# Kernel tuning notes

Hardware: AMD Instinct MI355X
Metric: run time of the kernel (lower is better)

The kernel has to match this reference:

```python
import jax, jax.numpy as jnp
import numpy as np

B, S, A, H, E = 8192, 256, 64, 1024, 8
IN = S + A
OUT = S + 1


def setup_inputs() -> dict:
    key = jax.random.key(0)
    ks = jax.random.split(key, 8)
    state = jax.random.normal(ks[0], (B, S), dtype=jnp.float32)
    action = jax.random.normal(ks[1], (B, A), dtype=jnp.float32)
    idx = jax.random.randint(ks[2], (B,), 0, E, dtype=jnp.int32)
    # Kaiming-ish scaling to keep activations sane
    W1 = jax.random.normal(ks[3], (E, IN, H), dtype=jnp.float32) / np.sqrt(IN)
    b1 = jnp.zeros((E, H), dtype=jnp.float32)
    W2 = jax.random.normal(ks[4], (E, H, H), dtype=jnp.float32) / np.sqrt(H)
    b2 = jnp.zeros((E, H), dtype=jnp.float32)
    W3 = jax.random.normal(ks[5], (E, H, OUT), dtype=jnp.float32) / np.sqrt(H)
    b3 = jnp.zeros((E, OUT), dtype=jnp.float32)
    return {"state": state, "action": action, "idx": idx,
            "W1": W1, "b1": b1, "W2": W2, "b2": b2, "W3": W3, "b3": b3}


def reference(state, action, idx, W1, b1, W2, b2, W3, b3):
    # Dense-MoE style: run all E experts on the full batch, then select the
    # per-sample expert output chosen by idx (matches masked gather/scatter
    # in the torch predict loop).
    x = jnp.concatenate([state, action], axis=-1)                  # [B, IN]
    h = jax.nn.relu(jnp.einsum('bi,eih->beh', x, W1) + b1)         # [B, E, H]
    h = jax.nn.relu(jnp.einsum('beh,ehk->bek', h, W2) + b2)        # [B, E, H]
    out = jnp.einsum('beh,eho->beo', h, W3) + b3                   # [B, E, S+1]
    sel = jnp.take_along_axis(out, idx[:, None, None], axis=1)[:, 0]  # [B, S+1]
    s_dim = state.shape[-1]
    delta = sel[:, :s_dim]
    reward = sel[:, s_dim:]
    next_state = state + delta
    return next_state, reward
```

## Files before the change

kernel.cpp:

```cpp
#include <hip/hip_runtime.h>
#include <stdint.h>

#define B_SZ   8192
#define IN_DIM 320
#define H_DIM  1024
#define E_NUM  8
#define OUT_DIM 257
#define TM     128
#define MAXT   (B_SZ / TM + E_NUM)
#define W3ROWS 384

typedef __bf16 bf16x8 __attribute__((ext_vector_type(8)));
typedef float  f32x4  __attribute__((ext_vector_type(4)));

typedef unsigned int __attribute__((address_space(1))) as1_uint;
typedef unsigned int __attribute__((address_space(3))) as3_uint;

__device__ __forceinline__ void gload_lds16(const void* g, void* l) {
    __builtin_amdgcn_global_load_lds((const as1_uint*)g, (as3_uint*)l, 16, 0, 0);
}

__device__ __forceinline__ unsigned short f2bf(float f) {
    unsigned int u = __float_as_uint(f);
    return (unsigned short)((u + 0x7fffu + ((u >> 16) & 1u)) >> 16);
}

__global__ __launch_bounds__(256)
void k_prep(const float* __restrict__ state, const float* __restrict__ action,
            const int* __restrict__ idx,
            const float* __restrict__ W1, const float* __restrict__ W2,
            const float* __restrict__ W3,
            unsigned short* __restrict__ xb, unsigned short* __restrict__ w1t,
            unsigned short* __restrict__ w2t, unsigned short* __restrict__ w3t,
            int* __restrict__ order, int* __restrict__ te,
            int* __restrict__ tp0, int* __restrict__ tcnt) {
    __shared__ float tile[64][65];
    __shared__ int scnt[16][E_NUM];
    int bid = blockIdx.x, tid = threadIdx.x;

    if (bid == 0) {
        int shard = tid & 15;
        if (tid < 128) ((int*)scnt)[tid] = 0;
        __syncthreads();
        for (int b = tid; b < B_SZ; b += 256) atomicAdd(&scnt[shard][idx[b]], 1);
        __syncthreads();
        if (tid == 0) {
            int pos = 0, tt = 0;
            for (int e = 0; e < E_NUM; e++) {
                int start = pos;
                for (int s = 0; s < 16; s++) { int c = scnt[s][e]; scnt[s][e] = pos; pos += c; }
                int tot = pos - start;
                for (int st = 0; st < tot; st += TM) {
                    te[tt] = e; tp0[tt] = start + st; tcnt[tt] = min(TM, tot - st); tt++;
                }
            }
            for (; tt < MAXT; tt++) { te[tt] = 0; tp0[tt] = 0; tcnt[tt] = 0; }
        }
        __syncthreads();
        for (int b = tid; b < B_SZ; b += 256) {
            int e = idx[b];
            int p = atomicAdd(&scnt[shard][e], 1);
            order[p] = b;
        }
        return;
    }

    if (bid <= 2560) {
        int q = (bid - 1) * 256 + tid;
        int b = q / 80, j = q % 80;
        float4 v = (j < 64) ? ((const float4*)state)[b * 64 + j]
                            : ((const float4*)action)[b * 16 + (j - 64)];
        ushort4 o;
        o.x = f2bf(v.x); o.y = f2bf(v.y); o.z = f2bf(v.z); o.w = f2bf(v.w);
        ((ushort4*)xb)[q] = o;
        return;
    }

    if (bid < 5761) {
        int e, kt, nt, K, Nsrc, dstRows;
        const float* src; unsigned short* dst;
        if (bid < 3201) {
            int r = bid - 2561; e = r / 80; int m = r % 80; kt = m / 16; nt = m % 16;
            K = IN_DIM; Nsrc = H_DIM; dstRows = H_DIM; src = W1; dst = w1t;
        } else if (bid < 5249) {
            int r = bid - 3201; e = r / 256; int m = r % 256; kt = m / 16; nt = m % 16;
            K = H_DIM; Nsrc = H_DIM; dstRows = H_DIM; src = W2; dst = w2t;
        } else {
            int r = bid - 5249; e = r / 64; int m = r % 64; kt = m / 4; nt = m % 4;
            K = H_DIM; Nsrc = OUT_DIM; dstRows = W3ROWS; src = W3; dst = w3t;
        }
        int k0 = kt * 64, n0 = nt * 64;
        const float* s = src + (size_t)e * K * Nsrc;
        unsigned short* d = dst + (size_t)e * dstRows * K;
        int tx = tid & 63, ty = tid >> 6;
        for (int rr = ty; rr < 64; rr += 4)
            tile[rr][tx] = s[(size_t)(k0 + rr) * Nsrc + (n0 + tx)];
        __syncthreads();
        for (int rr = ty; rr < 64; rr += 4)
            d[(size_t)(n0 + rr) * K + (k0 + tx)] = f2bf(tile[tx][rr]);
        return;
    }

    int i = (bid - 5761) * 256 + tid;
    int e = i >> 10, k = i & 1023;
    w3t[((size_t)e * W3ROWS + 256) * H_DIM + k] =
        f2bf(W3[((size_t)e * H_DIM + k) * OUT_DIM + 256]);
}

template <int K, bool GATHER, int MODE>
__global__ __launch_bounds__(256, 2)
void k_gemm(const unsigned short* __restrict__ Abase,
            const unsigned short* __restrict__ Wt, int wtRows,
            const float* __restrict__ bias, int bstride,
            unsigned short* __restrict__ Hout,
            float* __restrict__ Out, const float* __restrict__ state,
            const int* __restrict__ order,
            const int* __restrict__ te, const int* __restrict__ tp0,
            const int* __restrict__ tcnt) {
    constexpr int NI  = K / 32;
    constexpr int ABY = 128 * 64;
    constexpr int STG = 2 * ABY;
    __shared__ __align__(16) char lds[2 * STG];

    int t = blockIdx.x;
    int cnt = tcnt[t];
    if (cnt == 0) return;
    int e = te[t], p0 = tp0[t];
    int n0 = blockIdx.y * 128;
    int tid = threadIdx.x;
    int w = tid >> 6, lane = tid & 63;

    int r  = tid >> 2;
    int cg = (tid & 3) ^ ((r >> 1) & 3);
    int rc0 = r < cnt ? r : cnt - 1;
    int rc1 = (r + 64) < cnt ? (r + 64) : cnt - 1;
    long ar0 = GATHER ? order[p0 + rc0] : (p0 + rc0);
    long ar1 = GATHER ? order[p0 + rc1] : (p0 + rc1);
    const unsigned short* aP0 = Abase + (size_t)ar0 * K + cg * 8;
    const unsigned short* aP1 = Abase + (size_t)ar1 * K + cg * 8;
    const unsigned short* bP0 = Wt + ((size_t)e * wtRows + n0 + r) * K + cg * 8;
    const unsigned short* bP1 = bP0 + (size_t)64 * K;

    auto stage = [&](int k0, int sb) {
        gload_lds16(aP0 + k0, lds + sb + tid * 16);
        gload_lds16(aP1 + k0, lds + sb + 4096 + tid * 16);
        gload_lds16(bP0 + k0, lds + sb + ABY + tid * 16);
        gload_lds16(bP1 + k0, lds + sb + ABY + 4096 + tid * 16);
    };

    f32x4 acc[4][4];
#pragma unroll
    for (int i = 0; i < 4; i++)
#pragma unroll
        for (int j = 0; j < 4; j++) acc[i][j] = (f32x4)0.f;

    const int m_off = (w >> 1) * 64, n_off = (w & 1) * 64;
    const int fm   = lane & 15;
    const int kc   = lane >> 4;
    const int koff = (kc ^ ((fm >> 1) & 3)) * 8;

    stage(0, 0);
    for (int it = 0; it < NI; ++it) {
        __syncthreads();
        if (it + 1 < NI) stage((it + 1) * 32, ((it + 1) & 1) * STG);
        const unsigned short* As = (const unsigned short*)(lds + (it & 1) * STG);
        const unsigned short* Bs = As + ABY / 2;

        bf16x8 af[4], bf[4];
#pragma unroll
        for (int i = 0; i < 4; i++)
            af[i] = *(const bf16x8*)&As[(m_off + i * 16 + fm) * 32 + koff];
#pragma unroll
        for (int j = 0; j < 4; j++)
            bf[j] = *(const bf16x8*)&Bs[(n_off + j * 16 + fm) * 32 + koff];
#pragma unroll
        for (int i = 0; i < 4; i++)
#pragma unroll
            for (int j = 0; j < 4; j++)
                acc[i][j] = __builtin_amdgcn_mfma_f32_16x16x32_bf16(
                    af[i], bf[j], acc[i][j], 0, 0, 0);
    }

    int col = lane & 15, rq = lane >> 4;
#pragma unroll
    for (int j = 0; j < 4; j++) {
        int n = n0 + n_off + j * 16 + col;
        float bv = (MODE == 0) ? bias[e * bstride + n]
                               : ((n <= 256) ? bias[e * bstride + n] : 0.f);
#pragma unroll
        for (int i = 0; i < 4; i++) {
#pragma unroll
            for (int rr = 0; rr < 4; rr++) {
                int m = m_off + i * 16 + rq * 4 + rr;
                if (m < cnt) {
                    float v = acc[i][j][rr] + bv;
                    if (MODE == 0) {
                        Hout[(size_t)(p0 + m) * H_DIM + n] = f2bf(fmaxf(v, 0.f));
                    } else {
                        int row = order[p0 + m];
                        if (n < 256) {
                            size_t o = (size_t)row * 256 + n;
                            Out[o] = state[o] + v;
                        } else if (n == 256) {
                            Out[(size_t)B_SZ * 256 + row] = v;
                        }
                    }
                }
            }
        }
    }
}

extern "C" void kernel_launch(void* const* d_in, const int* in_sizes, int n_in,
                              void* d_out, int out_size, void* d_ws, size_t ws_size,
                              hipStream_t stream) {
    const float* state  = (const float*)d_in[0];
    const float* action = (const float*)d_in[1];
    const int*   idx    = (const int*)d_in[2];
    const float* W1     = (const float*)d_in[3];
    const float* b1     = (const float*)d_in[4];
    const float* W2     = (const float*)d_in[5];
    const float* b2     = (const float*)d_in[6];
    const float* W3     = (const float*)d_in[7];
    const float* b3     = (const float*)d_in[8];
    float* out = (float*)d_out;

    char* ws = (char*)d_ws;
    size_t off = 0;
    auto alloc = [&](size_t bytes) -> void* {
        void* p = ws + off;
        off = (off + bytes + 255) & ~(size_t)255;
        return p;
    };
    unsigned short* xb  = (unsigned short*)alloc((size_t)B_SZ * IN_DIM * 2);
    unsigned short* w1t = (unsigned short*)alloc((size_t)E_NUM * H_DIM * IN_DIM * 2);
    unsigned short* w2t = (unsigned short*)alloc((size_t)E_NUM * H_DIM * H_DIM * 2);
    unsigned short* w3t = (unsigned short*)alloc((size_t)E_NUM * W3ROWS * H_DIM * 2);
    unsigned short* h1  = (unsigned short*)alloc((size_t)B_SZ * H_DIM * 2);
    unsigned short* h2  = (unsigned short*)alloc((size_t)B_SZ * H_DIM * 2);
    int* order = (int*)alloc(B_SZ * 4);
    int* te    = (int*)alloc(MAXT * 4);
    int* tp0   = (int*)alloc(MAXT * 4);
    int* tcnt  = (int*)alloc(MAXT * 4);

    k_prep<<<5793, 256, 0, stream>>>(state, action, idx, W1, W2, W3,
                                     xb, w1t, w2t, w3t, order, te, tp0, tcnt);

    k_gemm<IN_DIM, true, 0><<<dim3(MAXT, 8), 256, 0, stream>>>(
        xb, w1t, H_DIM, b1, H_DIM, h1, nullptr, nullptr, order, te, tp0, tcnt);
    k_gemm<H_DIM, false, 0><<<dim3(MAXT, 8), 256, 0, stream>>>(
        h1, w2t, H_DIM, b2, H_DIM, h2, nullptr, nullptr, order, te, tp0, tcnt);
    k_gemm<H_DIM, false, 1><<<dim3(MAXT, 3), 256, 0, stream>>>(
        h2, w3t, W3ROWS, b3, OUT_DIM, nullptr, out, state, order, te, tp0, tcnt);
}
```

Baseline: 236.8 us.

## Shrink GEMM tiles to 64x64 single-wave blocks and overlap W2/W3 conversion with layer 1

Result: slower. 272.4 us (+15.0%).

```diff
diff --git a/kernel.cpp b/kernel.cpp
--- a/kernel.cpp
+++ b/kernel.cpp
@@ -6,9 +6,12 @@
 #define H_DIM  1024
 #define E_NUM  8
 #define OUT_DIM 257
-#define TM     128
+#define TM     64
 #define MAXT   (B_SZ / TM + E_NUM)
-#define W3ROWS 384
+#define W3ROWS 320
+#define NG12   (MAXT * 16)
+#define NG3    (MAXT * 5)
+#define NAUX   2568
 
 typedef __bf16 bf16x8 __attribute__((ext_vector_type(8)));
 typedef float  f32x4  __attribute__((ext_vector_type(4)));
@@ -25,16 +28,37 @@
     return (unsigned short)((u + 0x7fffu + ((u >> 16) & 1u)) >> 16);
 }
 
+__device__ __forceinline__ void trans64(const float* __restrict__ src,
+                                        unsigned short* __restrict__ dst,
+                                        int Ks, int Ns, int dR, int e, int kt,
+                                        int nt, unsigned short* sh,
+                                        int tid, int nthr) {
+    int k0 = kt * 64, n0 = nt * 64;
+    const float* s = src + (size_t)e * Ks * Ns + (size_t)k0 * Ns + n0;
+    unsigned short* d = dst + ((size_t)e * dR + n0) * Ks + k0;
+    int tx = tid & 63, wv = tid >> 6, nw = nthr >> 6;
+    for (int rr = wv; rr < 64; rr += nw)
+        sh[rr * 66 + tx] = f2bf(s[(size_t)rr * Ns + tx]);
+    __syncthreads();
+    int kq = tid & 15, nr = (tid >> 4) & 3;
+    for (int p = 0; p < 16 / nw; p++) {
+        int n = (wv + p * nw) * 4 + nr;
+        ushort4 o;
+        o.x = sh[(kq * 4 + 0) * 66 + n];
+        o.y = sh[(kq * 4 + 1) * 66 + n];
+        o.z = sh[(kq * 4 + 2) * 66 + n];
+        o.w = sh[(kq * 4 + 3) * 66 + n];
+        *(ushort4*)&d[(size_t)n * Ks + kq * 4] = o;
+    }
+}
+
 __global__ __launch_bounds__(256)
-void k_prep(const float* __restrict__ state, const float* __restrict__ action,
-            const int* __restrict__ idx,
-            const float* __restrict__ W1, const float* __restrict__ W2,
-            const float* __restrict__ W3,
-            unsigned short* __restrict__ xb, unsigned short* __restrict__ w1t,
-            unsigned short* __restrict__ w2t, unsigned short* __restrict__ w3t,
-            int* __restrict__ order, int* __restrict__ te,
-            int* __restrict__ tp0, int* __restrict__ tcnt) {
-    __shared__ float tile[64][65];
+void k_prep0(const float* __restrict__ state, const float* __restrict__ action,
+             const int* __restrict__ idx, const float* __restrict__ W1,
+             unsigned short* __restrict__ xb, unsigned short* __restrict__ w1t,
+             int* __restrict__ order, int* __restrict__ te,
+             int* __restrict__ tp0, int* __restrict__ tcnt) {
+    __shared__ unsigned short sh[64 * 66];
     __shared__ int scnt[16][E_NUM];
     int bid = blockIdx.x, tid = threadIdx.x;
 
@@ -65,50 +89,29 @@
         return;
     }
 
-    if (bid <= 2560) {
-        int q = (bid - 1) * 256 + tid;
-        int b = q / 80, j = q % 80;
-        float4 v = (j < 64) ? ((const float4*)state)[b * 64 + j]
-                            : ((const float4*)action)[b * 16 + (j - 64)];
-        ushort4 o;
-        o.x = f2bf(v.x); o.y = f2bf(v.y); o.z = f2bf(v.z); o.w = f2bf(v.w);
-        ((ushort4*)xb)[q] = o;
+    if (bid <= 320) {
+        int a = bid - 1;
+        const float4* sf = (const float4*)state;
+        const float4* af = (const float4*)action;
+#pragma unroll
+        for (int p = 0; p < 8; p++) {
+            int q = a * 2048 + p * 256 + tid;
+            int b = q / 80, j = q % 80;
+            float4 v = (j < 64) ? sf[b * 64 + j] : af[b * 16 + (j - 64)];
+            ushort4 o;
+            o.x = f2bf(v.x); o.y = f2bf(v.y); o.z = f2bf(v.z); o.w = f2bf(v.w);
+            ((ushort4*)xb)[q] = o;
+        }
         return;
     }
 
-    if (bid < 5761) {
-        int e, kt, nt, K, Nsrc, dstRows;
-        const float* src; unsigned short* dst;
-        if (bid < 3201) {
-            int r = bid - 2561; e = r / 80; int m = r % 80; kt = m / 16; nt = m % 16;
-            K = IN_DIM; Nsrc = H_DIM; dstRows = H_DIM; src = W1; dst = w1t;
-        } else if (bid < 5249) {
-            int r = bid - 3201; e = r / 256; int m = r % 256; kt = m / 16; nt = m % 16;
-            K = H_DIM; Nsrc = H_DIM; dstRows = H_DIM; src = W2; dst = w2t;
-        } else {
-            int r = bid - 5249; e = r / 64; int m = r % 64; kt = m / 4; nt = m % 4;
-            K = H_DIM; Nsrc = OUT_DIM; dstRows = W3ROWS; src = W3; dst = w3t;
-        }
-        int k0 = kt * 64, n0 = nt * 64;
-        const float* s = src + (size_t)e * K * Nsrc;
-        unsigned short* d = dst + (size_t)e * dstRows * K;
-        int tx = tid & 63, ty = tid >> 6;
-        for (int rr = ty; rr < 64; rr += 4)
-            tile[rr][tx] = s[(size_t)(k0 + rr) * Nsrc + (n0 + tx)];
-        __syncthreads();
-        for (int rr = ty; rr < 64; rr += 4)
-            d[(size_t)(n0 + rr) * K + (k0 + tx)] = f2bf(tile[tx][rr]);
-        return;
-    }
-
-    int i = (bid - 5761) * 256 + tid;
-    int e = i >> 10, k = i & 1023;
-    w3t[((size_t)e * W3ROWS + 256) * H_DIM + k] =
-        f2bf(W3[((size_t)e * H_DIM + k) * OUT_DIM + 256]);
-}
-
-template <int K, bool GATHER, int MODE>
-__global__ __launch_bounds__(256, 2)
+    int c = bid - 321;
+    int e = c / 80, m = c % 80, kt = m / 16, nt = m % 16;
+    trans64(W1, w1t, IN_DIM, H_DIM, H_DIM, e, kt, nt, sh, tid, 256);
+}
+
+template <int K, bool GATHER, int MODE, bool AUX>
+__global__ __launch_bounds__(64, 2)
 void k_gemm(const unsigned short* __restrict__ Abase,
             const unsigned short* __restrict__ Wt, int wtRows,
             const float* __restrict__ bias, int bstride,
@@ -116,36 +119,58 @@
             float* __restrict__ Out, const float* __restrict__ state,
             const int* __restrict__ order,
             const int* __restrict__ te, const int* __restrict__ tp0,
-            const int* __restrict__ tcnt) {
-    constexpr int NI  = K / 32;
-    constexpr int ABY = 128 * 64;
-    constexpr int STG = 2 * ABY;
-    __shared__ __align__(16) char lds[2 * STG];
-
-    int t = blockIdx.x;
+            const int* __restrict__ tcnt, int ng,
+            const float* __restrict__ W2, unsigned short* __restrict__ w2t,
+            const float* __restrict__ W3, unsigned short* __restrict__ w3t) {
+    __shared__ __align__(16) char lds[16384];
+    int bid = blockIdx.x, lane = threadIdx.x;
+
+    if (AUX && bid >= ng) {
+        int a = bid - ng;
+        if (a < 2048) {
+            trans64(W2, w2t, H_DIM, H_DIM, H_DIM, a >> 8, (a & 255) >> 4, a & 15,
+                    (unsigned short*)lds, lane, 64);
+        } else if (a < 2560) {
+            int b = a - 2048;
+            trans64(W3, w3t, H_DIM, OUT_DIM, W3ROWS, b >> 6, (b & 63) >> 2, b & 3,
+                    (unsigned short*)lds, lane, 64);
+        } else {
+            int e = a - 2560;
+#pragma unroll
+            for (int p = 0; p < 16; p++) {
+                int k = p * 64 + lane;
+                w3t[((size_t)e * W3ROWS + 256) * H_DIM + k] =
+                    f2bf(W3[((size_t)e * H_DIM + k) * OUT_DIM + 256]);
+            }
+        }
+        return;
+    }
+
+    int t = bid % MAXT, ny = bid / MAXT;
     int cnt = tcnt[t];
     if (cnt == 0) return;
     int e = te[t], p0 = tp0[t];
-    int n0 = blockIdx.y * 128;
-    int tid = threadIdx.x;
-    int w = tid >> 6, lane = tid & 63;
-
-    int r  = tid >> 2;
-    int cg = (tid & 3) ^ ((r >> 1) & 3);
-    int rc0 = r < cnt ? r : cnt - 1;
-    int rc1 = (r + 64) < cnt ? (r + 64) : cnt - 1;
-    long ar0 = GATHER ? order[p0 + rc0] : (p0 + rc0);
-    long ar1 = GATHER ? order[p0 + rc1] : (p0 + rc1);
-    const unsigned short* aP0 = Abase + (size_t)ar0 * K + cg * 8;
-    const unsigned short* aP1 = Abase + (size_t)ar1 * K + cg * 8;
-    const unsigned short* bP0 = Wt + ((size_t)e * wtRows + n0 + r) * K + cg * 8;
-    const unsigned short* bP1 = bP0 + (size_t)64 * K;
-
+    int n0 = ny * 64;
+    constexpr int NI = K / 32;
+
+    int r  = lane >> 2;
+    int cg = (lane & 3) ^ ((r >> 1) & 3);
+    const unsigned short* aP[4];
+    const unsigned short* bP[4];
+#pragma unroll
+    for (int g = 0; g < 4; g++) {
+        int rm = g * 16 + r;
+        int rc = rm < cnt ? rm : cnt - 1;
+        long ar = GATHER ? order[p0 + rc] : (p0 + rc);
+        aP[g] = Abase + (size_t)ar * K + cg * 8;
+        bP[g] = Wt + ((size_t)e * wtRows + n0 + rm) * K + cg * 8;
+    }
     auto stage = [&](int k0, int sb) {
-        gload_lds16(aP0 + k0, lds + sb + tid * 16);
-        gload_lds16(aP1 + k0, lds + sb + 4096 + tid * 16);
-        gload_lds16(bP0 + k0, lds + sb + ABY + tid * 16);
-        gload_lds16(bP1 + k0, lds + sb + ABY + 4096 + tid * 16);
+#pragma unroll
+        for (int g = 0; g < 4; g++) {
+            gload_lds16(aP[g] + k0, lds + sb + g * 1024 + lane * 16);
+            gload_lds16(bP[g] + k0, lds + sb + 4096 + g * 1024 + lane * 16);
+        }
     };
 
     f32x4 acc[4][4];
@@ -154,25 +179,23 @@
 #pragma unroll
         for (int j = 0; j < 4; j++) acc[i][j] = (f32x4)0.f;
 
-    const int m_off = (w >> 1) * 64, n_off = (w & 1) * 64;
     const int fm   = lane & 15;
-    const int kc   = lane >> 4;
-    const int koff = (kc ^ ((fm >> 1) & 3)) * 8;
+    const int koff = ((lane >> 4) ^ ((fm >> 1) & 3)) * 8;
 
     stage(0, 0);
     for (int it = 0; it < NI; ++it) {
         __syncthreads();
-        if (it + 1 < NI) stage((it + 1) * 32, ((it + 1) & 1) * STG);
-        const unsigned short* As = (const unsigned short*)(lds + (it & 1) * STG);
-        const unsigned short* Bs = As + ABY / 2;
+        if (it + 1 < NI) stage((it + 1) * 32, ((it + 1) & 1) * 8192);
+        const unsigned short* As = (const unsigned short*)(lds + (it & 1) * 8192);
+        const unsigned short* Bs = As + 2048;
 
         bf16x8 af[4], bf[4];
 #pragma unroll
         for (int i = 0; i < 4; i++)
-            af[i] = *(const bf16x8*)&As[(m_off + i * 16 + fm) * 32 + koff];
+            af[i] = *(const bf16x8*)&As[(i * 16 + fm) * 32 + koff];
 #pragma unroll
         for (int j = 0; j < 4; j++)
-            bf[j] = *(const bf16x8*)&Bs[(n_off + j * 16 + fm) * 32 + koff];
+            bf[j] = *(const bf16x8*)&Bs[(j * 16 + fm) * 32 + koff];
 #pragma unroll
         for (int i = 0; i < 4; i++)
 #pragma unroll
@@ -184,14 +207,14 @@
     int col = lane & 15, rq = lane >> 4;
 #pragma unroll
     for (int j = 0; j < 4; j++) {
-        int n = n0 + n_off + j * 16 + col;
+        int n = n0 + j * 16 + col;
         float bv = (MODE == 0) ? bias[e * bstride + n]
                                : ((n <= 256) ? bias[e * bstride + n] : 0.f);
 #pragma unroll
         for (int i = 0; i < 4; i++) {
 #pragma unroll
             for (int rr = 0; rr < 4; rr++) {
-                int m = m_off + i * 16 + rq * 4 + rr;
+                int m = i * 16 + rq * 4 + rr;
                 if (m < cnt) {
                     float v = acc[i][j][rr] + bv;
                     if (MODE == 0) {
@@ -243,13 +266,16 @@
     int* tp0   = (int*)alloc(MAXT * 4);
     int* tcnt  = (int*)alloc(MAXT * 4);
 
-    k_prep<<<5793, 256, 0, stream>>>(state, action, idx, W1, W2, W3,
-                                     xb, w1t, w2t, w3t, order, te, tp0, tcnt);
-
-    k_gemm<IN_DIM, true, 0><<<dim3(MAXT, 8), 256, 0, stream>>>(
-        xb, w1t, H_DIM, b1, H_DIM, h1, nullptr, nullptr, order, te, tp0, tcnt);
-    k_gemm<H_DIM, false, 0><<<dim3(MAXT, 8), 256, 0, stream>>>(
-        h1, w2t, H_DIM, b2, H_DIM, h2, nullptr, nullptr, order, te, tp0, tcnt);
-    k_gemm<H_DIM, false, 1><<<dim3(MAXT, 3), 256, 0, stream>>>(
-        h2, w3t, W3ROWS, b3, OUT_DIM, nullptr, out, state, order, te, tp0, tcnt);
-}
+    k_prep0<<<961, 256, 0, stream>>>(state, action, idx, W1, xb, w1t,
+                                     order, te, tp0, tcnt);
+
+    k_gemm<IN_DIM, true, 0, true><<<NG12 + NAUX, 64, 0, stream>>>(
+        xb, w1t, H_DIM, b1, H_DIM, h1, nullptr, nullptr, order, te, tp0, tcnt,
+        NG12, W2, w2t, W3, w3t);
+    k_gemm<H_DIM, false, 0, false><<<NG12, 64, 0, stream>>>(
+        h1, w2t, H_DIM, b2, H_DIM, h2, nullptr, nullptr, order, te, tp0, tcnt,
+        NG12, nullptr, nullptr, nullptr, nullptr);
+    k_gemm<H_DIM, false, 1, false><<<NG3, 64, 0, stream>>>(
+        h2, w3t, W3ROWS, b3, OUT_DIM, nullptr, out, state, order, te, tp0, tcnt,
+        NG3, nullptr, nullptr, nullptr, nullptr);
+}
```

## Vectorize weight transpose, move routing block last, interleave expert tiles in GEMM grid

Applied to the files above, without the earlier changes.

After: 239.3 us. Within noise of the previous version (+1.1%).

```diff
diff --git a/kernel.cpp b/kernel.cpp
--- a/kernel.cpp
+++ b/kernel.cpp
@@ -7,7 +7,7 @@
 #define E_NUM  8
 #define OUT_DIM 257
 #define TM     128
-#define MAXT   (B_SZ / TM + E_NUM)
+#define MT_MAX 64
 #define W3ROWS 384
 
 typedef __bf16 bf16x8 __attribute__((ext_vector_type(8)));
@@ -23,6 +23,46 @@
 __device__ __forceinline__ unsigned short f2bf(float f) {
     unsigned int u = __float_as_uint(f);
     return (unsigned short)((u + 0x7fffu + ((u >> 16) & 1u)) >> 16);
+}
+
+template <bool VEC>
+__device__ __forceinline__ void trans64(const float* __restrict__ src,
+                                        unsigned short* __restrict__ dst,
+                                        int Ks, int Ns, int dR, int e, int kt,
+                                        int nt, unsigned short* sh, int tid) {
+    int k0 = kt * 64, n0 = nt * 64;
+    const float* s = src + (size_t)e * Ks * Ns + (size_t)k0 * Ns + n0;
+    unsigned short* d = dst + ((size_t)e * dR + n0) * Ks + k0;
+    if (VEC) {
+        int c4 = tid & 15;
+#pragma unroll
+        for (int p = 0; p < 4; p++) {
+            int r = (tid >> 4) + p * 16;
+            float4 v = *(const float4*)&s[(size_t)r * Ns + c4 * 4];
+            ushort4 o;
+            o.x = f2bf(v.x); o.y = f2bf(v.y); o.z = f2bf(v.z); o.w = f2bf(v.w);
+            *(ushort4*)&sh[r * 66 + c4 * 4] = o;
+        }
+    } else {
+        int tx = tid & 63;
+#pragma unroll
+        for (int p = 0; p < 16; p++) {
+            int r = (tid >> 6) + p * 4;
+            sh[r * 66 + tx] = f2bf(s[(size_t)r * Ns + tx]);
+        }
+    }
+    __syncthreads();
+    int kq = tid & 15;
+#pragma unroll
+    for (int p = 0; p < 4; p++) {
+        int n = (tid >> 4) + p * 16;
+        ushort4 o;
+        o.x = sh[(kq * 4 + 0) * 66 + n];
+        o.y = sh[(kq * 4 + 1) * 66 + n];
+        o.z = sh[(kq * 4 + 2) * 66 + n];
+        o.w = sh[(kq * 4 + 3) * 66 + n];
+        *(ushort4*)&d[(size_t)n * Ks + kq * 4] = o;
+    }
 }
 
 __global__ __launch_bounds__(256)
@@ -32,79 +72,72 @@
             const float* __restrict__ W3,
             unsigned short* __restrict__ xb, unsigned short* __restrict__ w1t,
             unsigned short* __restrict__ w2t, unsigned short* __restrict__ w3t,
-            int* __restrict__ order, int* __restrict__ te,
-            int* __restrict__ tp0, int* __restrict__ tcnt) {
-    __shared__ float tile[64][65];
+            int* __restrict__ order, int* __restrict__ ebase,
+            int* __restrict__ etot) {
+    __shared__ unsigned short sh[64 * 66];
     __shared__ int scnt[16][E_NUM];
     int bid = blockIdx.x, tid = threadIdx.x;
 
-    if (bid == 0) {
-        int shard = tid & 15;
-        if (tid < 128) ((int*)scnt)[tid] = 0;
-        __syncthreads();
-        for (int b = tid; b < B_SZ; b += 256) atomicAdd(&scnt[shard][idx[b]], 1);
-        __syncthreads();
-        if (tid == 0) {
-            int pos = 0, tt = 0;
-            for (int e = 0; e < E_NUM; e++) {
-                int start = pos;
-                for (int s = 0; s < 16; s++) { int c = scnt[s][e]; scnt[s][e] = pos; pos += c; }
-                int tot = pos - start;
-                for (int st = 0; st < tot; st += TM) {
-                    te[tt] = e; tp0[tt] = start + st; tcnt[tt] = min(TM, tot - st); tt++;
-                }
-            }
-            for (; tt < MAXT; tt++) { te[tt] = 0; tp0[tt] = 0; tcnt[tt] = 0; }
-        }
-        __syncthreads();
-        for (int b = tid; b < B_SZ; b += 256) {
-            int e = idx[b];
-            int p = atomicAdd(&scnt[shard][e], 1);
-            order[p] = b;
-        }
-        return;
-    }
-
-    if (bid <= 2560) {
-        int q = (bid - 1) * 256 + tid;
-        int b = q / 80, j = q % 80;
-        float4 v = (j < 64) ? ((const float4*)state)[b * 64 + j]
-                            : ((const float4*)action)[b * 16 + (j - 64)];
-        ushort4 o;
-        o.x = f2bf(v.x); o.y = f2bf(v.y); o.z = f2bf(v.z); o.w = f2bf(v.w);
-        ((ushort4*)xb)[q] = o;
-        return;
-    }
-
-    if (bid < 5761) {
-        int e, kt, nt, K, Nsrc, dstRows;
-        const float* src; unsigned short* dst;
-        if (bid < 3201) {
-            int r = bid - 2561; e = r / 80; int m = r % 80; kt = m / 16; nt = m % 16;
-            K = IN_DIM; Nsrc = H_DIM; dstRows = H_DIM; src = W1; dst = w1t;
-        } else if (bid < 5249) {
-            int r = bid - 3201; e = r / 256; int m = r % 256; kt = m / 16; nt = m % 16;
-            K = H_DIM; Nsrc = H_DIM; dstRows = H_DIM; src = W2; dst = w2t;
-        } else {
-            int r = bid - 5249; e = r / 64; int m = r % 64; kt = m / 4; nt = m % 4;
-            K = H_DIM; Nsrc = OUT_DIM; dstRows = W3ROWS; src = W3; dst = w3t;
-        }
-        int k0 = kt * 64, n0 = nt * 64;
-        const float* s = src + (size_t)e * K * Nsrc;
-        unsigned short* d = dst + (size_t)e * dstRows * K;
-        int tx = tid & 63, ty = tid >> 6;
-        for (int rr = ty; rr < 64; rr += 4)
-            tile[rr][tx] = s[(size_t)(k0 + rr) * Nsrc + (n0 + tx)];
-        __syncthreads();
-        for (int rr = ty; rr < 64; rr += 4)
-            d[(size_t)(n0 + rr) * K + (k0 + tx)] = f2bf(tile[tx][rr]);
-        return;
-    }
-
-    int i = (bid - 5761) * 256 + tid;
-    int e = i >> 10, k = i & 1023;
-    w3t[((size_t)e * W3ROWS + 256) * H_DIM + k] =
-        f2bf(W3[((size_t)e * H_DIM + k) * OUT_DIM + 256]);
+    if (bid < 2048) {
+        int e = bid & 7, t = bid >> 3;
+        trans64<true>(W2, w2t, H_DIM, H_DIM, H_DIM, e, t >> 4, t & 15, sh, tid);
+        return;
+    }
+    if (bid < 2688) {
+        int a = bid - 2048, e = a & 7, t = a >> 3;
+        trans64<true>(W1, w1t, IN_DIM, H_DIM, H_DIM, e, t / 16, t % 16, sh, tid);
+        return;
+    }
+    if (bid < 3200) {
+        int a = bid - 2688, e = a & 7, t = a >> 3;
+        trans64<false>(W3, w3t, H_DIM, OUT_DIM, W3ROWS, e, t >> 2, t & 3, sh, tid);
+        return;
+    }
+    if (bid < 3520) {
+        int a = bid - 3200;
+        const float4* sf = (const float4*)state;
+        const float4* af = (const float4*)action;
+#pragma unroll
+        for (int p = 0; p < 8; p++) {
+            int q = a * 2048 + p * 256 + tid;
+            int b = q / 80, j = q % 80;
+            float4 v = (j < 64) ? sf[b * 64 + j] : af[b * 16 + (j - 64)];
+            ushort4 o;
+            o.x = f2bf(v.x); o.y = f2bf(v.y); o.z = f2bf(v.z); o.w = f2bf(v.w);
+            ((ushort4*)xb)[q] = o;
+        }
+        return;
+    }
+    if (bid < 3528) {
+        int e = bid - 3520;
+#pragma unroll
+        for (int p = 0; p < 4; p++) {
+            int k = p * 256 + tid;
+            w3t[((size_t)e * W3ROWS + 256) * H_DIM + k] =
+                f2bf(W3[((size_t)e * H_DIM + k) * OUT_DIM + 256]);
+        }
+        return;
+    }
+
+    int shard = tid & 15;
+    if (tid < 128) ((int*)scnt)[tid] = 0;
+    __syncthreads();
+    for (int b = tid; b < B_SZ; b += 256) atomicAdd(&scnt[shard][idx[b]], 1);
+    __syncthreads();
+    if (tid == 0) {
+        int pos = 0;
+        for (int e = 0; e < E_NUM; e++) {
+            int start = pos;
+            for (int s = 0; s < 16; s++) { int c = scnt[s][e]; scnt[s][e] = pos; pos += c; }
+            ebase[e] = start; etot[e] = pos - start;
+        }
+    }
+    __syncthreads();
+    for (int b = tid; b < B_SZ; b += 256) {
+        int e = idx[b];
+        int p = atomicAdd(&scnt[shard][e], 1);
+        order[p] = b;
+    }
 }
 
 template <int K, bool GATHER, int MODE>
@@ -115,18 +148,20 @@
             unsigned short* __restrict__ Hout,
             float* __restrict__ Out, const float* __restrict__ state,
             const int* __restrict__ order,
-            const int* __restrict__ te, const int* __restrict__ tp0,
-            const int* __restrict__ tcnt) {
+            const int* __restrict__ ebase, const int* __restrict__ etot) {
     constexpr int NI  = K / 32;
     constexpr int ABY = 128 * 64;
     constexpr int STG = 2 * ABY;
     __shared__ __align__(16) char lds[2 * STG];
 
-    int t = blockIdx.x;
-    int cnt = tcnt[t];
-    if (cnt == 0) return;
-    int e = te[t], p0 = tp0[t];
-    int n0 = blockIdx.y * 128;
+    int bid = blockIdx.x;
+    int e = bid & 7, rr_ = bid >> 3;
+    int mt = rr_ & (MT_MAX - 1), nt = rr_ >> 6;
+    int p0 = ebase[e] + mt * TM;
+    int cnt = etot[e] - mt * TM;
+    if (cnt <= 0) return;
+    cnt = cnt < TM ? cnt : TM;
+    int n0 = nt * 128;
     int tid = threadIdx.x;
     int w = tid >> 6, lane = tid & 63;
 
@@ -156,8 +191,7 @@
 
     const int m_off = (w >> 1) * 64, n_off = (w & 1) * 64;
     const int fm   = lane & 15;
-    const int kc   = lane >> 4;
-    const int koff = (kc ^ ((fm >> 1) & 3)) * 8;
+    const int koff = ((lane >> 4) ^ ((fm >> 1) & 3)) * 8;
 
     stage(0, 0);
     for (int it = 0; it < NI; ++it) {
@@ -239,17 +273,16 @@
     unsigned short* h1  = (unsigned short*)alloc((size_t)B_SZ * H_DIM * 2);
     unsigned short* h2  = (unsigned short*)alloc((size_t)B_SZ * H_DIM * 2);
     int* order = (int*)alloc(B_SZ * 4);
-    int* te    = (int*)alloc(MAXT * 4);
-    int* tp0   = (int*)alloc(MAXT * 4);
-    int* tcnt  = (int*)alloc(MAXT * 4);
-
-    k_prep<<<5793, 256, 0, stream>>>(state, action, idx, W1, W2, W3,
-                                     xb, w1t, w2t, w3t, order, te, tp0, tcnt);
-
-    k_gemm<IN_DIM, true, 0><<<dim3(MAXT, 8), 256, 0, stream>>>(
-        xb, w1t, H_DIM, b1, H_DIM, h1, nullptr, nullptr, order, te, tp0, tcnt);
-    k_gemm<H_DIM, false, 0><<<dim3(MAXT, 8), 256, 0, stream>>>(
-        h1, w2t, H_DIM, b2, H_DIM, h2, nullptr, nullptr, order, te, tp0, tcnt);
-    k_gemm<H_DIM, false, 1><<<dim3(MAXT, 3), 256, 0, stream>>>(
-        h2, w3t, W3ROWS, b3, OUT_DIM, nullptr, out, state, order, te, tp0, tcnt);
-}
+    int* ebase = (int*)alloc(E_NUM * 4);
+    int* etot  = (int*)alloc(E_NUM * 4);
+
+    k_prep<<<3529, 256, 0, stream>>>(state, action, idx, W1, W2, W3,
+                                     xb, w1t, w2t, w3t, order, ebase, etot);
+
+    k_gemm<IN_DIM, true, 0><<<8 * MT_MAX * 8, 256, 0, stream>>>(
+        xb, w1t, H_DIM, b1, H_DIM, h1, nullptr, nullptr, order, ebase, etot);
+    k_gemm<H_DIM, false, 0><<<8 * MT_MAX * 8, 256, 0, stream>>>(
+        h1, w2t, H_DIM, b2, H_DIM, h2, nullptr, nullptr, order, ebase, etot);
+    k_gemm<H_DIM, false, 1><<<8 * MT_MAX * 3, 256, 0, stream>>>(
+        h2, w3t, W3ROWS, b3, OUT_DIM, nullptr, out, state, order, ebase, etot);
+}
```
